# Optimization experiments

Measured on AMD Instinct MI355X. Metric: run time of the kernel, lower is better.

## Reference

```python
import jax, jax.numpy as jnp
import numpy as np

H = 16
D_MODEL = 1024
D_K = D_MODEL // H


def setup_inputs() -> dict:
    key = jax.random.key(0)
    ks = jax.random.split(key, 12)
    B, S = 4, 2048
    scale = 1.0 / np.sqrt(D_MODEL)
    inp = {
        "query": jax.random.normal(ks[0], (B, S, D_MODEL), dtype=jnp.float32),
        "key": jax.random.normal(ks[1], (B, S, D_MODEL), dtype=jnp.float32),
        "value": jax.random.normal(ks[2], (B, S, D_MODEL), dtype=jnp.float32),
        "Wq": jax.random.normal(ks[3], (D_MODEL, D_MODEL), dtype=jnp.float32) * scale,
        "bq": jnp.zeros((D_MODEL,), dtype=jnp.float32),
        "Wk": jax.random.normal(ks[4], (D_MODEL, D_MODEL), dtype=jnp.float32) * scale,
        "bk": jnp.zeros((D_MODEL,), dtype=jnp.float32),
        "Wv": jax.random.normal(ks[5], (D_MODEL, D_MODEL), dtype=jnp.float32) * scale,
        "bv": jnp.zeros((D_MODEL,), dtype=jnp.float32),
        "Wo": jax.random.normal(ks[6], (D_MODEL, D_MODEL), dtype=jnp.float32) * scale,
        "bo": jnp.zeros((D_MODEL,), dtype=jnp.float32),
    }
    return inp


def reference(query, key, value, Wq, bq, Wk, bk, Wv, bv, Wo, bo):
    B, S, _ = query.shape
    # Linear projections (torch Linear: x @ W^T + b), then split heads -> [B,H,S,d_k]
    def proj(x, W, b):
        y = x @ W.T + b
        return y.reshape(B, S, H, D_K).transpose(0, 2, 1, 3)

    q = proj(query, Wq, bq)
    k = proj(key, Wk, bk)
    v = proj(value, Wv, bv)

    # Explicit QK^T / sqrt(d_k), softmax, AV (no mask; dropout = identity in eval)
    scores = jnp.einsum("bhqd,bhkd->bhqk", q, k) / jnp.sqrt(jnp.float32(D_K))
    attn = jax.nn.softmax(scores, axis=-1)
    x = jnp.einsum("bhqk,bhkd->bhqd", attn, v)

    # Merge heads and final output projection
    x = x.transpose(0, 2, 1, 3).reshape(B, S, H * D_K)
    return x @ Wo.T + bo
```

## Files before the change

kernel.cpp:

```cpp
#include <hip/hip_runtime.h>
#include <hip/hip_bf16.h>
#include <stdint.h>

#define BATCH 4
#define SEQ   2048
#define DM    1024
#define NH    16
#define DK    64
#define MROWS (BATCH * SEQ)

#define C1 0.1803368801111204f

typedef __attribute__((ext_vector_type(8))) short short8;
typedef __attribute__((ext_vector_type(4))) float f32x4;
typedef __attribute__((ext_vector_type(4))) float floatv4;
typedef __attribute__((ext_vector_type(4))) unsigned short us4;
typedef __attribute__((ext_vector_type(4))) unsigned int uint4v;

static __device__ __forceinline__ unsigned short f2bf(float f) {
    union { float f; uint32_t u; } c; c.f = f;
    uint32_t u = c.u;
    return (unsigned short)((u + 0x7fffu + ((u >> 16) & 1u)) >> 16);
}

static __device__ __forceinline__ unsigned int cvt_pk_bf16(float a, float b) {
    __hip_bfloat162 h = __float22bfloat162_rn(float2{a, b});
    unsigned int u; __builtin_memcpy(&u, &h, 4); return u;
}

static __device__ __forceinline__ float ex2(float x) { return __builtin_amdgcn_exp2f(x); }

#define AS1C(p) ((const __attribute__((address_space(1))) unsigned int*)(uintptr_t)(const void*)(p))
#define AS3(p)  ((__attribute__((address_space(3))) unsigned int*)(uintptr_t)(void*)(p))

__global__ __launch_bounds__(256) void cvt3_k(const float* __restrict__ a, const float* __restrict__ b,
                                              const float* __restrict__ c,
                                              unsigned short* __restrict__ oa, unsigned short* __restrict__ ob,
                                              unsigned short* __restrict__ oc) {
    const int z = blockIdx.y;
    const float* s = (z == 0) ? a : (z == 1) ? b : c;
    unsigned short* o = (z == 0) ? oa : (z == 1) ? ob : oc;
    int i = blockIdx.x * 256 + threadIdx.x;
    floatv4 v = ((const floatv4*)s)[i];
    us4 w; w.x = f2bf(v.x); w.y = f2bf(v.y); w.z = f2bf(v.z); w.w = f2bf(v.w);
    ((us4*)o)[i] = w;
}

__global__ __launch_bounds__(256) void cvt4_k(const float* __restrict__ a, const float* __restrict__ b,
                                              const float* __restrict__ c, const float* __restrict__ d,
                                              unsigned short* __restrict__ oa, unsigned short* __restrict__ ob,
                                              unsigned short* __restrict__ oc, unsigned short* __restrict__ od) {
    const int z = blockIdx.y;
    const float* s = (z == 0) ? a : (z == 1) ? b : (z == 2) ? c : d;
    unsigned short* o = (z == 0) ? oa : (z == 1) ? ob : (z == 2) ? oc : od;
    int i = blockIdx.x * 256 + threadIdx.x;
    floatv4 v = ((const floatv4*)s)[i];
    us4 w; w.x = f2bf(v.x); w.y = f2bf(v.y); w.z = f2bf(v.z); w.w = f2bf(v.w);
    ((us4*)o)[i] = w;
}

static __device__ __forceinline__ void gemm256_body(const unsigned short* __restrict__ A,
                                                    const unsigned short* __restrict__ Bw,
                                                    const float* __restrict__ bias,
                                                    void* __restrict__ out, int m0, int n0,
                                                    float scale, int mode) {
    constexpr int K = DM;
    constexpr int NK = K / 64;
    constexpr int NIT = NK / 2;

    const int tid = threadIdx.x;
    const int wave = tid >> 6, lane = tid & 63, quad = lane >> 4, l16 = lane & 15;
    const int wm = wave >> 2, wn = wave & 3;

    __shared__ alignas(16) unsigned short AsU[4 * 8192];
    __shared__ alignas(16) unsigned short BsU[4 * 8192];

    f32x4 acc[8][4];
    #pragma unroll
    for (int i = 0; i < 8; i++)
        #pragma unroll
        for (int j = 0; j < 4; j++) acc[i][j] = (f32x4){0.f, 0.f, 0.f, 0.f};

    const int sl   = (lane & 7) ^ (lane >> 3);
    const int grow = wave * 16 + (lane >> 3) * 2 + (sl >> 2);
    const int gc8  = (sl & 3) * 8;
    const unsigned short* Ag = A  + (size_t)(m0 + grow) * K + gc8;
    const unsigned short* Bg = Bw + (size_t)(n0 + grow) * K + gc8;

    const int sx8 = ((((l16 & 1) * 4 + quad) ^ (l16 >> 1)) * 8);
    const int la  = wm * 4096 + (l16 >> 1) * 64 + sx8;
    const int lb  = wn * 2048 + (l16 >> 1) * 64 + sx8;

    short8 af[8], bfr[4];

#define G256_STG(GP, LDSP, b, kh, kt)                                                     \
    {   _Pragma("unroll")                                                                 \
        for (int s_ = 0; s_ < 2; s_++)                                                    \
            __builtin_amdgcn_global_load_lds(                                             \
                AS1C(GP + (size_t)s_ * 128 * K + (kt) * 64 + (kh) * 32),                  \
                AS3(LDSP + ((b) * 2 + (kh)) * 8192 + s_ * 4096 + wave * 512), 16, 0, 0); }

#define G256_LD(b, kh)                                                                    \
    {   const int rg_ = ((b) * 2 + (kh)) * 8192;                                          \
        _Pragma("unroll")                                                                 \
        for (int mf_ = 0; mf_ < 8; mf_++) af[mf_] = *(const short8*)&AsU[rg_ + la + mf_ * 512]; \
        _Pragma("unroll")                                                                 \
        for (int nf_ = 0; nf_ < 4; nf_++) bfr[nf_] = *(const short8*)&BsU[rg_ + lb + nf_ * 512]; }

#define G256_MMA(nh)                                                                      \
    {   __builtin_amdgcn_s_setprio(1);                                                    \
        _Pragma("unroll")                                                                 \
        for (int mf_ = 0; mf_ < 8; mf_++) {                                               \
            acc[mf_][2*(nh)]   = __builtin_amdgcn_mfma_f32_16x16x32_bf16(af[mf_], bfr[2*(nh)],   acc[mf_][2*(nh)],   0, 0, 0); \
            acc[mf_][2*(nh)+1] = __builtin_amdgcn_mfma_f32_16x16x32_bf16(af[mf_], bfr[2*(nh)+1], acc[mf_][2*(nh)+1], 0, 0, 0); } \
        __builtin_amdgcn_s_setprio(0); }

#define G256_VM10 asm volatile("s_waitcnt vmcnt(10)" ::: "memory")
#define G256_VM0  asm volatile("s_waitcnt vmcnt(0)"  ::: "memory")
#define G256_LG0  { asm volatile("s_waitcnt lgkmcnt(0)" ::: "memory"); __builtin_amdgcn_sched_barrier(0); }
#define G256_BAR  __builtin_amdgcn_s_barrier()
#define G256_SB0  __builtin_amdgcn_sched_barrier(0)

    G256_STG(Ag, AsU, 0, 0, 0); G256_STG(Bg, BsU, 0, 0, 0);
    G256_STG(Ag, AsU, 0, 1, 0); G256_STG(Bg, BsU, 0, 1, 0);
    G256_STG(Ag, AsU, 1, 0, 1); G256_STG(Bg, BsU, 1, 0, 1);
    G256_STG(Ag, AsU, 1, 1, 1);

    #pragma unroll 1
    for (int i = 0; i < NIT - 1; ++i) {
        const int t2 = 2 * i + 2, t3 = 2 * i + 3;
        G256_VM10; G256_BAR; G256_SB0;
        G256_STG(Bg, BsU, 1, 1, 2 * i + 1);
        G256_LD(0, 0); G256_LG0; G256_MMA(0); G256_BAR;
        G256_STG(Ag, AsU, 0, 0, t2); G256_MMA(1);
        G256_VM10; G256_BAR; G256_SB0;
        G256_STG(Bg, BsU, 0, 0, t2);
        G256_LD(0, 1); G256_LG0; G256_MMA(0); G256_BAR;
        G256_STG(Ag, AsU, 0, 1, t2); G256_MMA(1);
        G256_VM10; G256_BAR; G256_SB0;
        G256_STG(Bg, BsU, 0, 1, t2);
        G256_LD(1, 0); G256_LG0; G256_MMA(0); G256_BAR;
        G256_STG(Ag, AsU, 1, 0, t3); G256_MMA(1);
        G256_VM10; G256_BAR; G256_SB0;
        G256_STG(Bg, BsU, 1, 0, t3);
        G256_LD(1, 1); G256_LG0; G256_MMA(0); G256_BAR;
        G256_STG(Ag, AsU, 1, 1, t3); G256_MMA(1);
    }
    G256_STG(Bg, BsU, 1, 1, NK - 1);
    G256_VM0; G256_BAR; G256_SB0;
    G256_LD(0, 0); G256_LG0; G256_MMA(0); G256_MMA(1);
    G256_LD(0, 1); G256_LG0; G256_MMA(0); G256_MMA(1);
    G256_LD(1, 0); G256_LG0; G256_MMA(0); G256_MMA(1);
    G256_LD(1, 1); G256_LG0; G256_MMA(0); G256_MMA(1);

#undef G256_STG
#undef G256_LD
#undef G256_MMA
#undef G256_VM10
#undef G256_VM0
#undef G256_LG0
#undef G256_BAR
#undef G256_SB0

    #pragma unroll
    for (int nf = 0; nf < 4; nf++) {
        const int n = n0 + wn * 64 + nf * 16 + l16;
        const float bv = bias[n];
        if (mode == 2) {
            const int bb = m0 >> 11;
            const int hh = n >> 6, dd = n & (DK - 1);
            unsigned short* obase = (unsigned short*)out
                                  + (((size_t)bb * NH + hh) * DK + dd) * SEQ
                                  + (m0 & (SEQ - 1)) + wm * 128 + quad * 8;
            #pragma unroll
            for (int mf = 0; mf < 8; mf++) {
                us4 w;
                #pragma unroll
                for (int r = 0; r < 4; r++) w[r] = f2bf(acc[mf][nf][r] + bv);
                *(us4*)(obase + (mf >> 1) * 32 + (mf & 1) * 4) = w;
            }
        } else {
            const int hh = n >> 6, dd = n & (DK - 1);
            #pragma unroll
            for (int mf = 0; mf < 8; mf++) {
                #pragma unroll
                for (int r = 0; r < 4; r++) {
                    const int mrow = m0 + wm * 128 + mf * 16 + quad * 4 + r;
                    float val = (acc[mf][nf][r] + bv) * scale;
                    if (mode == 0) {
                        int bb = mrow >> 11, ss = mrow & (SEQ - 1);
                        ((unsigned short*)out)[((((size_t)bb * NH + hh) * SEQ + ss) << 6) + dd] = f2bf(val);
                    } else {
                        ((float*)out)[(size_t)mrow * DM + n] = val;
                    }
                }
            }
        }
    }
}

__global__ __launch_bounds__(512, 1) void gemm_qkv_k(const unsigned short* qa, const unsigned short* ka,
                                                     const unsigned short* va, const unsigned short* wq,
                                                     const unsigned short* wk, const unsigned short* wv,
                                                     const float* bq, const float* bk, const float* bv,
                                                     unsigned short* qh, unsigned short* kh,
                                                     unsigned short* vtc) {
    const int z = blockIdx.z;
    const unsigned short* A = (z == 0) ? qa : (z == 1) ? ka : va;
    const unsigned short* W = (z == 0) ? wq : (z == 1) ? wk : wv;
    const float* bi = (z == 0) ? bq : (z == 1) ? bk : bv;
    void* o = (z == 0) ? (void*)qh : (z == 1) ? (void*)kh : (void*)vtc;
    const float sc = (z == 0) ? C1 : 1.0f;
    const int mode = (z == 2) ? 2 : 0;
    gemm256_body(A, W, bi, o, blockIdx.x * 256, blockIdx.y * 256, sc, mode);
}

__global__ __launch_bounds__(512, 1) void gemm_o_k(const unsigned short* xb, const unsigned short* wo,
                                                   const float* bo, float* out) {
    gemm256_body(xb, wo, bo, out, blockIdx.x * 256, blockIdx.y * 256, 1.0f, 1);
}

__global__ __launch_bounds__(256, 2) void flash_attn_k(const unsigned short* __restrict__ Qh,
                                                       const unsigned short* __restrict__ Kh,
                                                       const unsigned short* __restrict__ Vtc,
                                                       unsigned short* __restrict__ Xb) {
    const int tid = threadIdx.x;
    const int wave = tid >> 6, lane = tid & 63, quad = lane >> 4, l16 = lane & 15;
    const int h = blockIdx.y, b = blockIdx.z;
    const unsigned short* Qp = Qh  + (size_t)(b * NH + h) * SEQ * DK;
    const unsigned short* Kp = Kh  + (size_t)(b * NH + h) * SEQ * DK;
    const unsigned short* Vp = Vtc + (size_t)(b * NH + h) * DK * SEQ;
    const int q0 = blockIdx.x * 256 + wave * 64;

    __shared__ alignas(16) unsigned short kt[128][72];
    __shared__ alignas(16) unsigned short vt[64][136];

    short8 aq[4][2];
    #pragma unroll
    for (int m = 0; m < 4; m++)
        #pragma unroll
        for (int kk = 0; kk < 2; kk++)
            aq[m][kk] = *(const short8*)(Qp + (size_t)(q0 + m * 16 + l16) * DK + kk * 32 + quad * 8);

    short8 ones;
    #pragma unroll
    for (int j = 0; j < 8; j++) ones[j] = (short)0x3F80;

    f32x4 O[4][4];
    f32x4 lacc[4];
    #pragma unroll
    for (int m = 0; m < 4; m++) {
        #pragma unroll
        for (int db = 0; db < 4; db++) O[m][db] = (f32x4){0.f, 0.f, 0.f, 0.f};
        lacc[m] = (f32x4){0.f, 0.f, 0.f, 0.f};
    }

    const unsigned short* kgp = Kp + (size_t)(tid >> 3) * DK + (tid & 7) * 8;
    const unsigned short* vgp = Vp + (size_t)(tid >> 4) * SEQ + (tid & 15) * 8;
    unsigned short* kws = &kt[tid >> 3][(tid & 7) * 8];
    unsigned short* vws = &vt[tid >> 4][(tid & 15) * 8];

    short8 krg[4], vrg[4];
    #pragma unroll
    for (int it = 0; it < 4; it++) {
        krg[it] = *(const short8*)(kgp + (size_t)it * 32 * DK);
        vrg[it] = *(const short8*)(vgp + (size_t)it * 16 * SEQ);
    }
    kgp += (size_t)128 * DK;
    vgp += 128;

    for (int t0 = 0; t0 < SEQ; t0 += 128) {
        __syncthreads();
        #pragma unroll
        for (int it = 0; it < 4; it++) {
            *(short8*)(kws + it * 32 * 72) = krg[it];
            *(short8*)(vws + it * 16 * 136) = vrg[it];
        }
        #pragma unroll
        for (int it = 0; it < 4; it++) {
            krg[it] = *(const short8*)(kgp + (size_t)it * 32 * DK);
            vrg[it] = *(const short8*)(vgp + (size_t)it * 16 * SEQ);
        }
        kgp += (size_t)128 * DK;
        vgp += 128;
        asm volatile("s_waitcnt lgkmcnt(0)" ::: "memory");
        __builtin_amdgcn_s_barrier();
        __builtin_amdgcn_sched_barrier(0);

        #pragma unroll
        for (int t = 0; t < 4; t++) {
            f32x4 s[4][2];
            #pragma unroll
            for (int m = 0; m < 4; m++)
                #pragma unroll
                for (int sb = 0; sb < 2; sb++) s[m][sb] = (f32x4){0.f, 0.f, 0.f, 0.f};

            #pragma unroll
            for (int kk = 0; kk < 2; kk++) {
                short8 bk0 = *(const short8*)&kt[(t * 2    ) * 16 + l16][kk * 32 + quad * 8];
                short8 bk1 = *(const short8*)&kt[(t * 2 + 1) * 16 + l16][kk * 32 + quad * 8];
                #pragma unroll
                for (int m = 0; m < 4; m++) {
                    s[m][0] = __builtin_amdgcn_mfma_f32_16x16x32_bf16(bk0, aq[m][kk], s[m][0], 0, 0, 0);
                    s[m][1] = __builtin_amdgcn_mfma_f32_16x16x32_bf16(bk1, aq[m][kk], s[m][1], 0, 0, 0);
                }
            }

            short8 pa[4];
            #pragma unroll
            for (int m = 0; m < 4; m++) {
                uint4v pk;
                pk.x = cvt_pk_bf16(ex2(s[m][0][0]), ex2(s[m][0][1]));
                pk.y = cvt_pk_bf16(ex2(s[m][0][2]), ex2(s[m][0][3]));
                pk.z = cvt_pk_bf16(ex2(s[m][1][0]), ex2(s[m][1][1]));
                pk.w = cvt_pk_bf16(ex2(s[m][1][2]), ex2(s[m][1][3]));
                __builtin_memcpy(&pa[m], &pk, 16);
            }

            #pragma unroll
            for (int db = 0; db < 4; db++) {
                short8 vf = *(const short8*)&vt[db * 16 + l16][t * 32 + quad * 8];
                #pragma unroll
                for (int m = 0; m < 4; m++)
                    O[m][db] = __builtin_amdgcn_mfma_f32_16x16x32_bf16(pa[m], vf, O[m][db], 0, 0, 0);
            }
            #pragma unroll
            for (int m = 0; m < 4; m++)
                lacc[m] = __builtin_amdgcn_mfma_f32_16x16x32_bf16(pa[m], ones, lacc[m], 0, 0, 0);
        }
    }

    #pragma unroll
    for (int m = 0; m < 4; m++) {
        #pragma unroll
        for (int r = 0; r < 4; r++) {
            const float inv = 1.f / lacc[m][r];
            const int srow = q0 + m * 16 + quad * 4 + r;
            unsigned short* op = Xb + ((size_t)b * SEQ + srow) * DM + h * DK;
            #pragma unroll
            for (int db = 0; db < 4; db++)
                op[db * 16 + l16] = f2bf(O[m][db][r] * inv);
        }
    }
}

extern "C" void kernel_launch(void* const* d_in, const int* in_sizes, int n_in,
                              void* d_out, int out_size, void* d_ws, size_t ws_size,
                              hipStream_t stream) {
    const float* q_in = (const float*)d_in[0];
    const float* k_in = (const float*)d_in[1];
    const float* v_in = (const float*)d_in[2];
    const float* Wq   = (const float*)d_in[3];
    const float* bq   = (const float*)d_in[4];
    const float* Wk   = (const float*)d_in[5];
    const float* bk   = (const float*)d_in[6];
    const float* Wv   = (const float*)d_in[7];
    const float* bv   = (const float*)d_in[8];
    const float* Wo   = (const float*)d_in[9];
    const float* bo   = (const float*)d_in[10];

    const size_t MB = 1024ull * 1024ull;
    char* ws = (char*)d_ws;
    unsigned short* qa  = (unsigned short*)(ws +   0 * MB);
    unsigned short* ka  = (unsigned short*)(ws +  16 * MB);
    unsigned short* va  = (unsigned short*)(ws +  32 * MB);
    unsigned short* wqb = (unsigned short*)(ws +  48 * MB);
    unsigned short* wkb = (unsigned short*)(ws +  50 * MB);
    unsigned short* wvb = (unsigned short*)(ws +  52 * MB);
    unsigned short* wob = (unsigned short*)(ws +  54 * MB);
    unsigned short* qh  = (unsigned short*)(ws +  56 * MB);
    unsigned short* kh  = (unsigned short*)(ws +  72 * MB);
    unsigned short* vtc = (unsigned short*)(ws +  88 * MB);
    unsigned short* xb  = (unsigned short*)(ws + 104 * MB);

    cvt3_k<<<dim3(8192, 3), 256, 0, stream>>>(q_in, k_in, v_in, qa, ka, va);
    cvt4_k<<<dim3(1024, 4), 256, 0, stream>>>(Wq, Wk, Wv, Wo, wqb, wkb, wvb, wob);

    gemm_qkv_k<<<dim3(MROWS / 256, DM / 256, 3), 512, 0, stream>>>(qa, ka, va, wqb, wkb, wvb,
                                                                   bq, bk, bv, qh, kh, vtc);

    flash_attn_k<<<dim3(SEQ / 256, NH, BATCH), 256, 0, stream>>>(qh, kh, vtc, xb);

    gemm_o_k<<<dim3(MROWS / 256, DM / 256), 512, 0, stream>>>(xb, wob, bo, (float*)d_out);
}
```

Measured before the change: 341.0 us.

## Shrink GEMM tiles to 256x128 with simpler double-buffered K=32 pipeline

Replaces the 256x256 GEMM tile with its deep 4-stage, K=64 software pipeline by a 256x128 tile using K=32 steps and a plain two-buffer ping-pong. This cuts LDS and registers so launch bounds can request more blocks per CU and the grid doubles for better load balance. The cost is less data reuse per tile, which raises global/L2 traffic, and a full vmcnt(0) wait plus barrier on every step, which exposes load latency.

Measured after the change: 327.0 us. 4.1% less time.

```diff
diff --git a/kernel.cpp b/kernel.cpp
--- a/kernel.cpp
+++ b/kernel.cpp
@@ -59,108 +59,82 @@
     ((us4*)o)[i] = w;
 }
 
-static __device__ __forceinline__ void gemm256_body(const unsigned short* __restrict__ A,
-                                                    const unsigned short* __restrict__ Bw,
-                                                    const float* __restrict__ bias,
-                                                    void* __restrict__ out, int m0, int n0,
-                                                    float scale, int mode) {
+static __device__ __forceinline__ void gemm_body(const unsigned short* __restrict__ A,
+                                                 const unsigned short* __restrict__ Bw,
+                                                 const float* __restrict__ bias,
+                                                 void* __restrict__ out, int m0, int n0,
+                                                 float scale, int mode) {
     constexpr int K = DM;
-    constexpr int NK = K / 64;
-    constexpr int NIT = NK / 2;
+    constexpr int NK = K / 32;
 
     const int tid = threadIdx.x;
     const int wave = tid >> 6, lane = tid & 63, quad = lane >> 4, l16 = lane & 15;
-    const int wm = wave >> 2, wn = wave & 3;
-
-    __shared__ alignas(16) unsigned short AsU[4 * 8192];
-    __shared__ alignas(16) unsigned short BsU[4 * 8192];
-
-    f32x4 acc[8][4];
-    #pragma unroll
-    for (int i = 0; i < 8; i++)
+    const int wm = wave >> 1, wn = wave & 1;
+
+    __shared__ alignas(16) unsigned short As[2][256 * 32];
+    __shared__ alignas(16) unsigned short Bs[2][128 * 32];
+
+    f32x4 acc[4][4];
+    #pragma unroll
+    for (int i = 0; i < 4; i++)
         #pragma unroll
         for (int j = 0; j < 4; j++) acc[i][j] = (f32x4){0.f, 0.f, 0.f, 0.f};
 
-    const int sl   = (lane & 7) ^ (lane >> 3);
-    const int grow = wave * 16 + (lane >> 3) * 2 + (sl >> 2);
-    const int gc8  = (sl & 3) * 8;
-    const unsigned short* Ag = A  + (size_t)(m0 + grow) * K + gc8;
-    const unsigned short* Bg = Bw + (size_t)(n0 + grow) * K + gc8;
-
-    const int sx8 = ((((l16 & 1) * 4 + quad) ^ (l16 >> 1)) * 8);
-    const int la  = wm * 4096 + (l16 >> 1) * 64 + sx8;
-    const int lb  = wn * 2048 + (l16 >> 1) * 64 + sx8;
-
-    short8 af[8], bfr[4];
-
-#define G256_STG(GP, LDSP, b, kh, kt)                                                     \
+    const int scol8 = (((lane & 3) ^ ((lane >> 3) & 3))) * 8;
+    const unsigned short* Ag0 = A  + (size_t)(m0 + wave * 32 + (lane >> 2)) * K + scol8;
+    const unsigned short* Ag1 = Ag0 + (size_t)16 * K;
+    const unsigned short* Bg0 = Bw + (size_t)(n0 + wave * 16 + (lane >> 2)) * K + scol8;
+
+    const int rsw = (quad ^ ((l16 >> 1) & 3)) * 8;
+
+    short8 af[4], bfr[4];
+
+#define GX_STG(b, kt)                                                                     \
+    {   __builtin_amdgcn_global_load_lds(AS1C(Ag0 + (size_t)(kt) * 32),                   \
+                                         AS3(&As[b][(wave * 32) * 32]), 16, 0, 0);        \
+        __builtin_amdgcn_global_load_lds(AS1C(Ag1 + (size_t)(kt) * 32),                   \
+                                         AS3(&As[b][(wave * 32 + 16) * 32]), 16, 0, 0);   \
+        __builtin_amdgcn_global_load_lds(AS1C(Bg0 + (size_t)(kt) * 32),                   \
+                                         AS3(&Bs[b][(wave * 16) * 32]), 16, 0, 0); }
+
+#define GX_LD(b)                                                                          \
     {   _Pragma("unroll")                                                                 \
-        for (int s_ = 0; s_ < 2; s_++)                                                    \
-            __builtin_amdgcn_global_load_lds(                                             \
-                AS1C(GP + (size_t)s_ * 128 * K + (kt) * 64 + (kh) * 32),                  \
-                AS3(LDSP + ((b) * 2 + (kh)) * 8192 + s_ * 4096 + wave * 512), 16, 0, 0); }
-
-#define G256_LD(b, kh)                                                                    \
-    {   const int rg_ = ((b) * 2 + (kh)) * 8192;                                          \
+        for (int i_ = 0; i_ < 4; i_++) af[i_]  = *(const short8*)&As[b][(wm * 64 + i_ * 16 + l16) * 32 + rsw]; \
         _Pragma("unroll")                                                                 \
-        for (int mf_ = 0; mf_ < 8; mf_++) af[mf_] = *(const short8*)&AsU[rg_ + la + mf_ * 512]; \
-        _Pragma("unroll")                                                                 \
-        for (int nf_ = 0; nf_ < 4; nf_++) bfr[nf_] = *(const short8*)&BsU[rg_ + lb + nf_ * 512]; }
-
-#define G256_MMA(nh)                                                                      \
+        for (int j_ = 0; j_ < 4; j_++) bfr[j_] = *(const short8*)&Bs[b][(wn * 64 + j_ * 16 + l16) * 32 + rsw]; }
+
+#define GX_MMA                                                                            \
     {   __builtin_amdgcn_s_setprio(1);                                                    \
         _Pragma("unroll")                                                                 \
-        for (int mf_ = 0; mf_ < 8; mf_++) {                                               \
-            acc[mf_][2*(nh)]   = __builtin_amdgcn_mfma_f32_16x16x32_bf16(af[mf_], bfr[2*(nh)],   acc[mf_][2*(nh)],   0, 0, 0); \
-            acc[mf_][2*(nh)+1] = __builtin_amdgcn_mfma_f32_16x16x32_bf16(af[mf_], bfr[2*(nh)+1], acc[mf_][2*(nh)+1], 0, 0, 0); } \
+        for (int i_ = 0; i_ < 4; i_++)                                                    \
+            _Pragma("unroll")                                                             \
+            for (int j_ = 0; j_ < 4; j_++)                                                \
+                acc[i_][j_] = __builtin_amdgcn_mfma_f32_16x16x32_bf16(af[i_], bfr[j_], acc[i_][j_], 0, 0, 0); \
         __builtin_amdgcn_s_setprio(0); }
 
-#define G256_VM10 asm volatile("s_waitcnt vmcnt(10)" ::: "memory")
-#define G256_VM0  asm volatile("s_waitcnt vmcnt(0)"  ::: "memory")
-#define G256_LG0  { asm volatile("s_waitcnt lgkmcnt(0)" ::: "memory"); __builtin_amdgcn_sched_barrier(0); }
-#define G256_BAR  __builtin_amdgcn_s_barrier()
-#define G256_SB0  __builtin_amdgcn_sched_barrier(0)
-
-    G256_STG(Ag, AsU, 0, 0, 0); G256_STG(Bg, BsU, 0, 0, 0);
-    G256_STG(Ag, AsU, 0, 1, 0); G256_STG(Bg, BsU, 0, 1, 0);
-    G256_STG(Ag, AsU, 1, 0, 1); G256_STG(Bg, BsU, 1, 0, 1);
-    G256_STG(Ag, AsU, 1, 1, 1);
-
+#define GX_VM0  { asm volatile("s_waitcnt vmcnt(0)" ::: "memory"); }
+#define GX_BAR  __builtin_amdgcn_s_barrier()
+#define GX_SB0  __builtin_amdgcn_sched_barrier(0)
+#define GX_LG0  { asm volatile("s_waitcnt lgkmcnt(0)" ::: "memory"); __builtin_amdgcn_sched_barrier(0); }
+
+    GX_STG(0, 0);
     #pragma unroll 1
-    for (int i = 0; i < NIT - 1; ++i) {
-        const int t2 = 2 * i + 2, t3 = 2 * i + 3;
-        G256_VM10; G256_BAR; G256_SB0;
-        G256_STG(Bg, BsU, 1, 1, 2 * i + 1);
-        G256_LD(0, 0); G256_LG0; G256_MMA(0); G256_BAR;
-        G256_STG(Ag, AsU, 0, 0, t2); G256_MMA(1);
-        G256_VM10; G256_BAR; G256_SB0;
-        G256_STG(Bg, BsU, 0, 0, t2);
-        G256_LD(0, 1); G256_LG0; G256_MMA(0); G256_BAR;
-        G256_STG(Ag, AsU, 0, 1, t2); G256_MMA(1);
-        G256_VM10; G256_BAR; G256_SB0;
-        G256_STG(Bg, BsU, 0, 1, t2);
-        G256_LD(1, 0); G256_LG0; G256_MMA(0); G256_BAR;
-        G256_STG(Ag, AsU, 1, 0, t3); G256_MMA(1);
-        G256_VM10; G256_BAR; G256_SB0;
-        G256_STG(Bg, BsU, 1, 0, t3);
-        G256_LD(1, 1); G256_LG0; G256_MMA(0); G256_BAR;
-        G256_STG(Ag, AsU, 1, 1, t3); G256_MMA(1);
-    }
-    G256_STG(Bg, BsU, 1, 1, NK - 1);
-    G256_VM0; G256_BAR; G256_SB0;
-    G256_LD(0, 0); G256_LG0; G256_MMA(0); G256_MMA(1);
-    G256_LD(0, 1); G256_LG0; G256_MMA(0); G256_MMA(1);
-    G256_LD(1, 0); G256_LG0; G256_MMA(0); G256_MMA(1);
-    G256_LD(1, 1); G256_LG0; G256_MMA(0); G256_MMA(1);
-
-#undef G256_STG
-#undef G256_LD
-#undef G256_MMA
-#undef G256_VM10
-#undef G256_VM0
-#undef G256_LG0
-#undef G256_BAR
-#undef G256_SB0
+    for (int k = 0; k < NK; k += 2) {
+        GX_VM0; GX_BAR; GX_SB0;
+        GX_STG(1, k + 1);
+        GX_LD(0); GX_LG0; GX_MMA;
+        GX_VM0; GX_BAR; GX_SB0;
+        if (k + 2 < NK) GX_STG(0, k + 2);
+        GX_LD(1); GX_LG0; GX_MMA;
+    }
+
+#undef GX_STG
+#undef GX_LD
+#undef GX_MMA
+#undef GX_VM0
+#undef GX_BAR
+#undef GX_SB0
+#undef GX_LG0
 
     #pragma unroll
     for (int nf = 0; nf < 4; nf++) {
@@ -171,9 +145,9 @@
             const int hh = n >> 6, dd = n & (DK - 1);
             unsigned short* obase = (unsigned short*)out
                                   + (((size_t)bb * NH + hh) * DK + dd) * SEQ
-                                  + (m0 & (SEQ - 1)) + wm * 128 + quad * 8;
-            #pragma unroll
-            for (int mf = 0; mf < 8; mf++) {
+                                  + (m0 & (SEQ - 1)) + wm * 64 + quad * 8;
+            #pragma unroll
+            for (int mf = 0; mf < 4; mf++) {
                 us4 w;
                 #pragma unroll
                 for (int r = 0; r < 4; r++) w[r] = f2bf(acc[mf][nf][r] + bv);
@@ -182,10 +156,10 @@
         } else {
             const int hh = n >> 6, dd = n & (DK - 1);
             #pragma unroll
-            for (int mf = 0; mf < 8; mf++) {
+            for (int mf = 0; mf < 4; mf++) {
                 #pragma unroll
                 for (int r = 0; r < 4; r++) {
-                    const int mrow = m0 + wm * 128 + mf * 16 + quad * 4 + r;
+                    const int mrow = m0 + wm * 64 + mf * 16 + quad * 4 + r;
                     float val = (acc[mf][nf][r] + bv) * scale;
                     if (mode == 0) {
                         int bb = mrow >> 11, ss = mrow & (SEQ - 1);
@@ -199,7 +173,7 @@
     }
 }
 
-__global__ __launch_bounds__(512, 1) void gemm_qkv_k(const unsigned short* qa, const unsigned short* ka,
+__global__ __launch_bounds__(512, 4) void gemm_qkv_k(const unsigned short* qa, const unsigned short* ka,
                                                      const unsigned short* va, const unsigned short* wq,
                                                      const unsigned short* wk, const unsigned short* wv,
                                                      const float* bq, const float* bk, const float* bv,
@@ -212,12 +186,12 @@
     void* o = (z == 0) ? (void*)qh : (z == 1) ? (void*)kh : (void*)vtc;
     const float sc = (z == 0) ? C1 : 1.0f;
     const int mode = (z == 2) ? 2 : 0;
-    gemm256_body(A, W, bi, o, blockIdx.x * 256, blockIdx.y * 256, sc, mode);
-}
-
-__global__ __launch_bounds__(512, 1) void gemm_o_k(const unsigned short* xb, const unsigned short* wo,
+    gemm_body(A, W, bi, o, blockIdx.x * 256, blockIdx.y * 128, sc, mode);
+}
+
+__global__ __launch_bounds__(512, 4) void gemm_o_k(const unsigned short* xb, const unsigned short* wo,
                                                    const float* bo, float* out) {
-    gemm256_body(xb, wo, bo, out, blockIdx.x * 256, blockIdx.y * 256, 1.0f, 1);
+    gemm_body(xb, wo, bo, out, blockIdx.x * 256, blockIdx.y * 128, 1.0f, 1);
 }
 
 __global__ __launch_bounds__(256, 2) void flash_attn_k(const unsigned short* __restrict__ Qh,
@@ -376,10 +350,10 @@
     cvt3_k<<<dim3(8192, 3), 256, 0, stream>>>(q_in, k_in, v_in, qa, ka, va);
     cvt4_k<<<dim3(1024, 4), 256, 0, stream>>>(Wq, Wk, Wv, Wo, wqb, wkb, wvb, wob);
 
-    gemm_qkv_k<<<dim3(MROWS / 256, DM / 256, 3), 512, 0, stream>>>(qa, ka, va, wqb, wkb, wvb,
+    gemm_qkv_k<<<dim3(MROWS / 256, DM / 128, 3), 512, 0, stream>>>(qa, ka, va, wqb, wkb, wvb,
                                                                    bq, bk, bv, qh, kh, vtc);
 
     flash_attn_k<<<dim3(SEQ / 256, NH, BATCH), 256, 0, stream>>>(qh, kh, vtc, xb);
 
-    gemm_o_k<<<dim3(MROWS / 256, DM / 256), 512, 0, stream>>>(xb, wob, bo, (float*)d_out);
-}
+    gemm_o_k<<<dim3(MROWS / 256, DM / 128), 512, 0, stream>>>(xb, wob, bo, (float*)d_out);
+}
```
